# Optimization experiments

Hardware: AMD Instinct MI355X
Metric: run time of the kernel (lower is better)

The kernel has to match this reference:

```python
import jax, jax.numpy as jnp
import numpy as np
import math

B, N, DIN, H, D, M, K, E = 1, 30000, 128, 4, 64, 64, 6, 480000
TAU = 0.25
EPS = 1e-6  # numerical_stabilizer in softmax_kernel_transformation


def _make_projection(m, d, seed=0):
    # FAVOR+ projection: stacked QR-orthogonalized blocks, rows rescaled by
    # norms of iid gaussian rows (scaling == 0 branch of create_projection_matrix).
    rng = np.random.default_rng(seed)
    blocks, rows = [], 0
    while rows < m:
        q, _ = np.linalg.qr(rng.standard_normal((d, d)))
        blocks.append(q.T[: min(d, m - rows)])
        rows += d
    mat = np.vstack(blocks)
    mult = np.linalg.norm(rng.standard_normal((m, d)), axis=1)
    return jnp.asarray(mult[:, None] * mat, dtype=jnp.float32)


def setup_inputs() -> dict:
    key = jax.random.key(0)
    ks = jax.random.split(key, 10)
    f32 = jnp.float32
    return {
        "z": jax.random.normal(ks[0], (B, N, DIN), dtype=f32),
        "Wq_w": jax.random.normal(ks[1], (DIN, H * D), dtype=f32) * DIN ** -0.5,
        "Wq_b": jnp.zeros((H * D,), f32),
        "Wk_w": jax.random.normal(ks[2], (DIN, H * D), dtype=f32) * DIN ** -0.5,
        "Wk_b": jnp.zeros((H * D,), f32),
        "Wv_w": jax.random.normal(ks[3], (DIN, H * D), dtype=f32) * DIN ** -0.5,
        "Wv_b": jnp.zeros((H * D,), f32),
        "Wo_w": jax.random.normal(ks[4], (H * D, D), dtype=f32) * (H * D) ** -0.5,
        "Wo_b": jnp.zeros((D,), f32),
        "proj": _make_projection(M, D),
        "gumbels": jax.random.gumbel(ks[5], (N, B, H, K), dtype=f32),
        "edge_index": jax.random.randint(ks[6], (2, E), 0, N),
    }


def _softmax_kernel(data, proj, is_query):
    # softmax_kernel_transformation: positive random features for exp kernel.
    dn = 1.0 / jnp.sqrt(jnp.sqrt(jnp.asarray(data.shape[-1], data.dtype)))
    data = data * dn  # [B,N,H,D]
    ratio = 1.0 / jnp.sqrt(jnp.asarray(proj.shape[0], data.dtype))
    dd = jnp.einsum("bnhd,md->bnhm", data, proj)
    diag = jnp.sum(data * data, axis=-1, keepdims=True) * 0.5
    if is_query:
        mx = jnp.max(dd, axis=-1, keepdims=True)            # per-row max
    else:
        mx = jnp.max(dd, axis=(1, 3), keepdims=True)        # max over n and m
    return ratio * (jnp.exp(dd - diag - mx) + EPS)


def reference(z, Wq_w, Wq_b, Wk_w, Wk_b, Wv_w, Wv_b, Wo_w, Wo_b, proj, gumbels, edge_index):
    inv_sqrt_tau = 1.0 / math.sqrt(TAU)
    q = (z @ Wq_w + Wq_b).reshape(B, N, H, D) * inv_sqrt_tau
    k = (z @ Wk_w + Wk_b).reshape(B, N, H, D) * inv_sqrt_tau
    v = (z @ Wv_w + Wv_b).reshape(B, N, H, D)

    qp = jnp.transpose(_softmax_kernel(q, proj, True), (1, 0, 2, 3))   # [N,B,H,M]
    kp = jnp.transpose(_softmax_kernel(k, proj, False), (1, 0, 2, 3))  # [N,B,H,M]
    v = jnp.transpose(v, (1, 0, 2, 3))                                  # [N,B,H,D]

    g = gumbels / TAU                                                   # [N,B,H,K]
    kt = kp[:, :, :, None, :] * jnp.exp(g)[..., None]                   # [N,B,H,K,M]

    kvs = jnp.einsum("nbhkm,nbhd->bhkmd", kt, v)
    z_num = jnp.einsum("nbhm,bhkmd->nbhkd", qp, kvs)                    # [N,B,H,K,D]
    ks_sum = jnp.sum(kt, axis=0)                                        # [B,H,K,M]
    z_den = jnp.einsum("nbhm,bhkm->nbhk", qp, ks_sum)                   # [N,B,H,K]
    z_out = jnp.mean(z_num / z_den[..., None], axis=3)                  # [N,B,H,D]
    z_out = jnp.transpose(z_out, (1, 0, 2, 3))                          # [B,N,H,D]

    # edge attention weights (for edge loss), non-gumbel normalizer
    start, end = edge_index[0], edge_index[1]
    edge_num = jnp.einsum("ebhm,ebhm->ebh", qp[end], kp[start])         # [E,B,H]
    norm = jnp.einsum("nbhm,bhm->nbh", qp, jnp.sum(kp, axis=0))         # [N,B,H]
    A_weight = jnp.transpose(edge_num / norm[end], (1, 0, 2))           # [B,E,H]

    z_next = z_out.reshape(B, N, H * D) @ Wo_w + Wo_b                   # [B,N,D]
    return z_next, A_weight
```

## Files before the change

kernel.cpp:

```cpp
#include <hip/hip_runtime.h>
#include <hip/hip_bf16.h>

#define NN   30000
#define DIN  128
#define NHD  256
#define HH   4
#define DD   64
#define MM   64
#define KK   6
#define EE   480000
#define ZOFF 1920000
#define NCS   125
#define CHUNK 240
#define PITCH  30208
#define PITCH4 3776

typedef __attribute__((ext_vector_type(8))) short bf16x8;
typedef __attribute__((ext_vector_type(4))) float f32x4;
typedef __attribute__((ext_vector_type(2))) float f32x2;

__device__ __forceinline__ unsigned f2key(float f) {
    unsigned u = __float_as_uint(f);
    return (u & 0x80000000u) ? ~u : (u | 0x80000000u);
}
__device__ __forceinline__ float key2f(unsigned k) {
    return __uint_as_float((k & 0x80000000u) ? (k ^ 0x80000000u) : ~k);
}
__device__ __forceinline__ unsigned short f2bf(float f) {
    unsigned u = __float_as_uint(f);
    unsigned r = ((u >> 16) & 1u) + 0x7fffu;
    return (unsigned short)((u + r) >> 16);
}
__device__ __forceinline__ float bf2f(unsigned short u) {
    return __uint_as_float((unsigned)u << 16);
}
__device__ __forceinline__ unsigned char ftofp8(float x) {
    unsigned u = __float_as_uint(x);
    int e32 = (int)(u >> 23) - 127;
    if (e32 <= -7) {
        int m = (int)rintf(x * 512.f);
        return (unsigned char)m;
    }
    unsigned r = ((u >> 20) & 1u) + 0x7FFFFu;
    u += r;
    e32 = (int)(u >> 23) - 127;
    if (e32 > 8) return 0x7E;
    int m = (u >> 20) & 7;
    return (unsigned char)(((e32 + 7) << 3) | m);
}
__device__ __forceinline__ float fp8tof(unsigned char u) {
    int e = (u >> 3) & 15, m = u & 7;
    if (e == 0) return (float)m * 0.001953125f;
    return __uint_as_float((unsigned)((e + 120) << 23) | ((unsigned)m << 20));
}
__device__ __forceinline__ void fp8x4tof(unsigned w, float* o) {
#if __has_builtin(__builtin_amdgcn_cvt_pk_f32_fp8)
    f32x2 lo = __builtin_amdgcn_cvt_pk_f32_fp8((int)w, false);
    f32x2 hi = __builtin_amdgcn_cvt_pk_f32_fp8((int)w, true);
    o[0] = lo[0]; o[1] = lo[1]; o[2] = hi[0]; o[3] = hi[1];
#else
    o[0] = fp8tof((unsigned char)(w & 255));
    o[1] = fp8tof((unsigned char)((w >> 8) & 255));
    o[2] = fp8tof((unsigned char)((w >> 16) & 255));
    o[3] = fp8tof((unsigned char)((w >> 24) & 255));
#endif
}

__global__ void init_kernel(unsigned* gmax) {
    if (threadIdx.x < HH) gmax[threadIdx.x] = 0u;
}

__global__ __launch_bounds__(256) void zcast_kernel(
    const float* __restrict__ z, unsigned short* __restrict__ zh) {
    int idx = blockIdx.x * 256 + threadIdx.x;
    float4 v = ((const float4*)z)[idx];
    ushort4 u;
    u.x = f2bf(v.x); u.y = f2bf(v.y); u.z = f2bf(v.z); u.w = f2bf(v.w);
    ((ushort4*)zh)[idx] = u;
}

__global__ __launch_bounds__(256) void wtransp_kernel(
    const float* __restrict__ Wq, const float* __restrict__ Wk,
    const float* __restrict__ Wv, unsigned short* __restrict__ WT) {
    __shared__ unsigned short tl[64][72];
    const int t = threadIdx.x;
    const int kt = blockIdx.x & 1, ct = blockIdx.x >> 1;
    const int wi = blockIdx.y;
    const float* W = (wi == 0) ? Wq : (wi == 1) ? Wk : Wv;
    const float4* W4 = (const float4*)W;
    #pragma unroll
    for (int it = 0; it < 4; ++it) {
        int idx = t + it * 256;
        int r = idx >> 4, c4 = idx & 15;
        float4 v = W4[(kt * 64 + r) * 64 + ct * 16 + c4];
        tl[c4 * 4 + 0][r] = f2bf(v.x);
        tl[c4 * 4 + 1][r] = f2bf(v.y);
        tl[c4 * 4 + 2][r] = f2bf(v.z);
        tl[c4 * 4 + 3][r] = f2bf(v.w);
    }
    __syncthreads();
    uint4* d4 = (uint4*)WT;
    #pragma unroll
    for (int it = 0; it < 2; ++it) {
        int idx = t + it * 256;
        int m = idx >> 3, g = idx & 7;
        d4[((size_t)wi * 256 + ct * 64 + m) * 16 + kt * 8 + g] = *(uint4*)&tl[m][g * 8];
    }
}

__global__ void projcast_kernel(const float* __restrict__ proj,
                                unsigned short* __restrict__ projh) {
    int i = blockIdx.x * 256 + threadIdx.x;
    projh[i] = f2bf(proj[i] * 0.35355339059327373f);
}

__global__ __launch_bounds__(256) void qkv_mfma_kernel(
    const unsigned short* __restrict__ zh, const unsigned short* __restrict__ WT,
    const float* __restrict__ bq, const float* __restrict__ bk, const float* __restrict__ bv,
    unsigned short* __restrict__ qh, unsigned short* __restrict__ kh,
    unsigned short* __restrict__ vh) {
    __shared__ __align__(16) unsigned short zt[128 * 128];
    __shared__ __align__(16) unsigned short wt[64 * 128];
    const int t = threadIdx.x;
    const int n0 = blockIdx.x * 128;
    const int wi = blockIdx.y;
    const float sc = (wi == 2) ? 1.0f : 2.0f;
    const float* bias = (wi == 0) ? bq : (wi == 1) ? bk : bv;
    unsigned short* outp = (wi == 0) ? qh : (wi == 1) ? kh : vh;
    const uint4* zg = (const uint4*)zh;
    #pragma unroll
    for (int it = 0; it < 8; ++it) {
        int idx = t + it * 256;
        int row = idx >> 4, g = idx & 15;
        int n = n0 + row;
        uint4 v = make_uint4(0u, 0u, 0u, 0u);
        if (n < NN) v = zg[(size_t)n * 16 + g];
        *(uint4*)&zt[row * 128 + ((g ^ (row & 7)) * 8)] = v;
    }
    const uint4* wg = (const uint4*)WT + (size_t)wi * 4096;
    const int w = t >> 6, lane = t & 63, lrow = lane & 15, lk = lane >> 4;
    for (int cc = 0; cc < 4; ++cc) {
        __syncthreads();
        #pragma unroll
        for (int it = 0; it < 4; ++it) {
            int idx = t + it * 256;
            int r = idx >> 4, g = idx & 15;
            *(uint4*)&wt[r * 128 + ((g ^ (r & 7)) * 8)] = wg[(cc * 64 + r) * 16 + g];
        }
        __syncthreads();
        f32x4 acc[4][2];
        #pragma unroll
        for (int mt = 0; mt < 4; ++mt) {
            acc[mt][0] = (f32x4){0.f, 0.f, 0.f, 0.f};
            acc[mt][1] = (f32x4){0.f, 0.f, 0.f, 0.f};
        }
        #pragma unroll
        for (int ks = 0; ks < 4; ++ks) {
            const int g0 = ks * 4 + lk;
            bf16x8 a[4], b[2];
            #pragma unroll
            for (int mt = 0; mt < 4; ++mt) {
                int r = mt * 16 + lrow;
                a[mt] = *(const bf16x8*)&wt[r * 128 + ((g0 ^ (r & 7)) * 8)];
            }
            #pragma unroll
            for (int nt = 0; nt < 2; ++nt) {
                int node = (w * 2 + nt) * 16 + lrow;
                b[nt] = *(const bf16x8*)&zt[node * 128 + ((g0 ^ (node & 7)) * 8)];
            }
            #pragma unroll
            for (int mt = 0; mt < 4; ++mt)
                #pragma unroll
                for (int nt = 0; nt < 2; ++nt)
                    acc[mt][nt] = __builtin_amdgcn_mfma_f32_16x16x32_bf16(
                        a[mt], b[nt], acc[mt][nt], 0, 0, 0);
        }
        #pragma unroll
        for (int mt = 0; mt < 4; ++mt) {
            int cbase = cc * 64 + mt * 16 + lk * 4;
            float4 bi = *(const float4*)&bias[cbase];
            #pragma unroll
            for (int nt = 0; nt < 2; ++nt) {
                int n = n0 + (w * 2 + nt) * 16 + lrow;
                if (n < NN) {
                    ushort4 u;
                    u.x = f2bf((acc[mt][nt][0] + bi.x) * sc);
                    u.y = f2bf((acc[mt][nt][1] + bi.y) * sc);
                    u.z = f2bf((acc[mt][nt][2] + bi.z) * sc);
                    u.w = f2bf((acc[mt][nt][3] + bi.w) * sc);
                    *(ushort4*)&outp[(size_t)n * NHD + cbase] = u;
                }
            }
        }
    }
}

__global__ __launch_bounds__(256) void feat_mfma_kernel(
    unsigned short* __restrict__ qbh, const unsigned short* __restrict__ kh,
    float* __restrict__ kb, const unsigned short* __restrict__ projh,
    unsigned* __restrict__ gmax) {
    __shared__ __align__(16) unsigned short at[64 * 64];
    __shared__ __align__(16) unsigned short pb[64 * 64];
    __shared__ __align__(16) float ddt[64 * 68];
    __shared__ float diag_sh[64];
    __shared__ float wmax_sh[4];
    const int t = threadIdx.x;
    const int h = blockIdx.y;
    const int n0 = blockIdx.x * 64;
    const int tx = t & 15, ty = t >> 4;
    const uint4* pg = (const uint4*)projh;
    #pragma unroll
    for (int q = 0; q < 2; ++q) {
        int idx = t + q * 256;
        int m = idx >> 3, g = idx & 7;
        *(uint4*)&pb[m * 64 + ((g ^ (m & 7)) * 8)] = pg[idx];
    }
    const int w = t >> 6, lane = t & 63, lrow = lane & 15, lk = lane >> 4;
    const int arow = w * 16 + lrow;
    #pragma unroll
    for (int pass = 0; pass < 2; ++pass) {
        const uint4* src = (const uint4*)(pass ? kh : qbh);
        __syncthreads();
        #pragma unroll
        for (int q = 0; q < 2; ++q) {
            int idx = t + q * 256;
            int n = idx >> 3, g = idx & 7;
            uint4 v = make_uint4(0u, 0u, 0u, 0u);
            if (n0 + n < NN) v = src[(size_t)(n0 + n) * 32 + h * 8 + g];
            *(uint4*)&at[n * 64 + ((g ^ (n & 7)) * 8)] = v;
            const unsigned short* e8 = (const unsigned short*)&v;
            float ss = 0.f;
            #pragma unroll
            for (int j2 = 0; j2 < 8; ++j2) { float f = bf2f(e8[j2]); ss += f * f; }
            ss += __shfl_xor(ss, 1, 64);
            ss += __shfl_xor(ss, 2, 64);
            ss += __shfl_xor(ss, 4, 64);
            if (g == 0) diag_sh[n] = 0.0625f * ss;
        }
        __syncthreads();
        bf16x8 a0 = *(const bf16x8*)&at[arow * 64 + ((lk ^ (arow & 7)) * 8)];
        bf16x8 a1 = *(const bf16x8*)&at[arow * 64 + (((lk + 4) ^ (arow & 7)) * 8)];
        #pragma unroll
        for (int ct = 0; ct < 4; ++ct) {
            int brow = ct * 16 + lrow;
            bf16x8 b0 = *(const bf16x8*)&pb[brow * 64 + ((lk ^ (brow & 7)) * 8)];
            bf16x8 b1 = *(const bf16x8*)&pb[brow * 64 + (((lk + 4) ^ (brow & 7)) * 8)];
            f32x4 acc = {0.f, 0.f, 0.f, 0.f};
            acc = __builtin_amdgcn_mfma_f32_16x16x32_bf16(a0, b0, acc, 0, 0, 0);
            acc = __builtin_amdgcn_mfma_f32_16x16x32_bf16(a1, b1, acc, 0, 0, 0);
            #pragma unroll
            for (int r = 0; r < 4; ++r)
                ddt[(w * 16 + lk * 4 + r) * 68 + ct * 16 + lrow] = acc[r];
        }
        __syncthreads();
        if (pass == 0) {
            #pragma unroll
            for (int i = 0; i < 4; ++i) {
                int n = n0 + ty * 4 + i;
                float a_[4];
                #pragma unroll
                for (int j = 0; j < 4; ++j) a_[j] = ddt[(ty * 4 + i) * 68 + tx * 4 + j];
                float mx = fmaxf(fmaxf(a_[0], a_[1]), fmaxf(a_[2], a_[3]));
                mx = fmaxf(mx, __shfl_xor(mx, 1, 64));
                mx = fmaxf(mx, __shfl_xor(mx, 2, 64));
                mx = fmaxf(mx, __shfl_xor(mx, 4, 64));
                mx = fmaxf(mx, __shfl_xor(mx, 8, 64));
                if (n < NN) {
                    float dg = diag_sh[ty * 4 + i] + mx;
                    ushort4 u;
                    u.x = f2bf(0.125f * (__expf(a_[0] - dg) + 1e-6f));
                    u.y = f2bf(0.125f * (__expf(a_[1] - dg) + 1e-6f));
                    u.z = f2bf(0.125f * (__expf(a_[2] - dg) + 1e-6f));
                    u.w = f2bf(0.125f * (__expf(a_[3] - dg) + 1e-6f));
                    *(ushort4*)&qbh[(size_t)n * NHD + h * DD + tx * 4] = u;
                }
            }
        } else {
            float km = -3.4e38f;
            #pragma unroll
            for (int i = 0; i < 4; ++i) {
                int n = n0 + ty * 4 + i;
                if (n < NN) {
                    float a_[4];
                    #pragma unroll
                    for (int j = 0; j < 4; ++j) a_[j] = ddt[(ty * 4 + i) * 68 + tx * 4 + j];
                    float dg = diag_sh[ty * 4 + i];
                    float4 o;
                    o.x = a_[0] - dg; o.y = a_[1] - dg;
                    o.z = a_[2] - dg; o.w = a_[3] - dg;
                    *(float4*)&kb[(size_t)n * NHD + h * DD + tx * 4] = o;
                    km = fmaxf(km, fmaxf(fmaxf(a_[0], a_[1]), fmaxf(a_[2], a_[3])));
                }
            }
            #pragma unroll
            for (int off = 1; off < 64; off <<= 1) km = fmaxf(km, __shfl_xor(km, off, 64));
            if ((t & 63) == 0) wmax_sh[t >> 6] = km;
            __syncthreads();
            if (t == 0) {
                float m2 = fmaxf(fmaxf(wmax_sh[0], wmax_sh[1]), fmaxf(wmax_sh[2], wmax_sh[3]));
                atomicMax(&gmax[h], f2key(m2));
            }
        }
    }
}

__global__ __launch_bounds__(256) void kfin_tr_kernel(
    const float* __restrict__ kb, const unsigned* __restrict__ gmax,
    unsigned short* __restrict__ kbh, unsigned short* __restrict__ kbhT) {
    __shared__ unsigned short tl[64][72];
    const int t = threadIdx.x;
    const int n0 = blockIdx.x * 64;
    const int h = blockIdx.y;
    const float mx = key2f(gmax[h]);
    const float4* s4 = (const float4*)kb;
    #pragma unroll
    for (int it = 0; it < 4; ++it) {
        int idx = t + it * 256;
        int n = idx >> 4, c4 = idx & 15;
        ushort4 u = make_ushort4(0, 0, 0, 0);
        if (n0 + n < NN) {
            float4 v = s4[(size_t)(n0 + n) * 64 + h * 16 + c4];
            u.x = f2bf(0.125f * (__expf(v.x - mx) + 1e-6f));
            u.y = f2bf(0.125f * (__expf(v.y - mx) + 1e-6f));
            u.z = f2bf(0.125f * (__expf(v.z - mx) + 1e-6f));
            u.w = f2bf(0.125f * (__expf(v.w - mx) + 1e-6f));
            *(ushort4*)&kbh[(size_t)(n0 + n) * NHD + h * DD + c4 * 4] = u;
        }
        tl[c4 * 4 + 0][n] = u.x;
        tl[c4 * 4 + 1][n] = u.y;
        tl[c4 * 4 + 2][n] = u.z;
        tl[c4 * 4 + 3][n] = u.w;
    }
    __syncthreads();
    uint4* d4 = (uint4*)kbhT;
    #pragma unroll
    for (int it = 0; it < 2; ++it) {
        int idx = t + it * 256;
        int m = idx >> 3, g = idx & 7;
        d4[(size_t)(h * 64 + m) * PITCH4 + (n0 >> 3) + g] = *(uint4*)&tl[m][g * 8];
    }
}

__global__ __launch_bounds__(256) void transp_bf16_kernel(
    const unsigned short* __restrict__ src, unsigned short* __restrict__ dst) {
    __shared__ unsigned short tl[64][72];
    const int t = threadIdx.x;
    const int nt = blockIdx.x * 64;
    const int h = blockIdx.y;
    const uint4* s4 = (const uint4*)src;
    #pragma unroll
    for (int it = 0; it < 2; ++it) {
        int idx = t + it * 256;
        int n = idx >> 3, g = idx & 7;
        uint4 v = make_uint4(0u, 0u, 0u, 0u);
        if (nt + n < NN) v = s4[(size_t)(nt + n) * 32 + h * 8 + g];
        const unsigned short* e = (const unsigned short*)&v;
        #pragma unroll
        for (int j = 0; j < 8; ++j) tl[g * 8 + j][n] = e[j];
    }
    __syncthreads();
    uint4* d4 = (uint4*)dst;
    #pragma unroll
    for (int it = 0; it < 2; ++it) {
        int idx = t + it * 256;
        int m = idx >> 3, g = idx & 7;
        d4[(size_t)(h * 64 + m) * PITCH4 + (nt >> 3) + g] = *(uint4*)&tl[m][g * 8];
    }
}

__global__ __launch_bounds__(256) void fp8cast_kernel(
    const unsigned short* __restrict__ src, unsigned char* __restrict__ dst) {
    int idx = blockIdx.x * 256 + threadIdx.x;
    uint4 v = ((const uint4*)src)[idx];
    const unsigned short* e = (const unsigned short*)&v;
    unsigned char o[8];
    #pragma unroll
    for (int j = 0; j < 8; ++j) o[j] = ftofp8(bf2f(e[j]) * 2048.f);
    ((uint2*)dst)[idx] = *(uint2*)o;
}

__global__ __launch_bounds__(512) void kvs_kernel(
    const unsigned short* __restrict__ kbhT, const unsigned short* __restrict__ vbhT,
    const float* __restrict__ gum,
    unsigned short* __restrict__ kvsp, float* __restrict__ ksp, float* __restrict__ ksump) {
    __shared__ __align__(16) unsigned short va [64 * 64];
    __shared__ __align__(16) unsigned short kpw[KK][64 * 64];
    __shared__ float w_sh[KK][256];
    const int c = blockIdx.x, h = blockIdx.y;
    const int t = threadIdx.x;
    const int n0 = c * CHUNK;
    const int n1 = n0 + CHUNK;
    for (int i = t; i < 256; i += 512) {
        int n = n0 + i;
        bool ok = (i < CHUNK);
        #pragma unroll
        for (int k = 0; k < KK; ++k)
            w_sh[k][i] = ok ? __expf(gum[n * 24 + h * KK + k] * 4.0f) : 0.f;
    }
    const int m_ = t >> 3, g_ = t & 7;
    const int w = t >> 6, lane = t & 63, lrow = lane & 15, lk = lane >> 4;
    const int ds = w & 3, mh = w >> 2;
    const int arow = ds * 16 + lrow;
    f32x4 acc[KK][2];
    #pragma unroll
    for (int k = 0; k < KK; ++k) {
        acc[k][0] = (f32x4){0.f, 0.f, 0.f, 0.f};
        acc[k][1] = (f32x4){0.f, 0.f, 0.f, 0.f};
    }
    float ks_acc[KK] = {0.f, 0.f, 0.f, 0.f, 0.f, 0.f};
    float ksum_acc = 0.f;
    const uint4* kT4 = (const uint4*)kbhT;
    const uint4* vT4 = (const uint4*)vbhT;
    __syncthreads();
    #pragma unroll
    for (int s = 0; s < 4; ++s) {
        const int nb = n0 + s * 64;
        uint4 kvv = kT4[(size_t)(h * 64 + m_) * PITCH4 + (nb >> 3) + g_];
        uint4 vvv = vT4[(size_t)(h * 64 + m_) * PITCH4 + (nb >> 3) + g_];
        const int slot = g_ ^ (m_ & 7);
        *(uint4*)&va[m_ * 64 + slot * 8] = vvv;
        float kf[8];
        {
            const unsigned short* ke = (const unsigned short*)&kvv;
            float sl = 0.f;
            int nbase = nb + g_ * 8;
            #pragma unroll
            for (int e = 0; e < 8; ++e) {
                kf[e] = bf2f(ke[e]);
                if (nbase + e < n1) sl += kf[e];
            }
            sl += __shfl_xor(sl, 1, 64);
            sl += __shfl_xor(sl, 2, 64);
            sl += __shfl_xor(sl, 4, 64);
            if (g_ == 0) ksum_acc += sl;
        }
        const int bw = s * 64;
        const int gg = g_ ^ (m_ & 7);
        #pragma unroll
        for (int k = 0; k < KK; ++k) {
            unsigned short ov[8];
            float sl = 0.f;
            #pragma unroll
            for (int e = 0; e < 8; ++e) {
                float p = kf[e] * w_sh[k][bw + gg * 8 + e];
                sl += p;
                ov[e] = f2bf(p);
            }
            *(uint4*)&kpw[k][m_ * 64 + g_ * 8] = *(uint4*)ov;
            sl += __shfl_xor(sl, 1, 64);
            sl += __shfl_xor(sl, 2, 64);
            sl += __shfl_xor(sl, 4, 64);
            if (g_ == 0) ks_acc[k] += sl;
        }
        __syncthreads();
        bf16x8 a0 = *(const bf16x8*)&va[arow * 64 + ((lk ^ (arow & 7)) * 8)];
        bf16x8 a1 = *(const bf16x8*)&va[arow * 64 + (((lk + 4) ^ (arow & 7)) * 8)];
        #pragma unroll
        for (int k = 0; k < KK; ++k) {
            #pragma unroll
            for (int mt = 0; mt < 2; ++mt) {
                int m = (mh * 2 + mt) * 16 + lrow;
                bf16x8 b0 = *(const bf16x8*)&kpw[k][m * 64 + ((lk ^ (m & 7)) * 8)];
                bf16x8 b1 = *(const bf16x8*)&kpw[k][m * 64 + (((lk + 4) ^ (m & 7)) * 8)];
                acc[k][mt] = __builtin_amdgcn_mfma_f32_16x16x32_bf16(a0, b0, acc[k][mt], 0, 0, 0);
                acc[k][mt] = __builtin_amdgcn_mfma_f32_16x16x32_bf16(a1, b1, acc[k][mt], 0, 0, 0);
            }
        }
        __syncthreads();
    }
    const size_t cb = (size_t)(c * HH + h) * KK;
    #pragma unroll
    for (int k = 0; k < KK; ++k)
        #pragma unroll
        for (int mt = 0; mt < 2; ++mt) {
            int m = (mh * 2 + mt) * 16 + lrow;
            #pragma unroll
            for (int r = 0; r < 4; ++r) {
                int d = ds * 16 + lk * 4 + r;
                kvsp[(cb + k) * 4096 + d * 64 + m] = f2bf(acc[k][mt][r]);
            }
        }
    if (g_ == 0) {
        #pragma unroll
        for (int k = 0; k < KK; ++k)
            ksp[(cb + k) * 64 + m_] = ks_acc[k];
        ksump[(size_t)(c * HH + h) * 64 + m_] = ksum_acc;
    }
}

__global__ void reduce_kernel(const unsigned short* __restrict__ kvsp,
                              const float* __restrict__ ksp, const float* __restrict__ ksump,
                              unsigned short* __restrict__ kvshT, float* __restrict__ kss,
                              float* __restrict__ ksum) {
    int idx = blockIdx.x * 256 + threadIdx.x;
    if (idx < 98304) {
        float s = 0.f;
        for (int c = 0; c < NCS; ++c) s += bf2f(kvsp[c * 98304 + idx]);
        kvshT[idx] = f2bf(s);
    } else if (idx < 98304 + 1536) {
        int o = idx - 98304;
        float s = 0.f;
        for (int c = 0; c < NCS; ++c) s += ksp[c * 1536 + o];
        kss[o] = s;
    } else if (idx < 98304 + 1536 + 256) {
        int o = idx - 98304 - 1536;
        float s = 0.f;
        for (int c = 0; c < NCS; ++c) s += ksump[c * 256 + o];
        ksum[o] = s;
    }
}

__global__ __launch_bounds__(256) void znum_kernel(
    const unsigned short* __restrict__ qbh, const unsigned short* __restrict__ kvshT,
    const float* __restrict__ kss, const float* __restrict__ ksum,
    unsigned short* __restrict__ zouth, float* __restrict__ nrm) {
    __shared__ __align__(16) unsigned short qpa[64 * 64];
    __shared__ __align__(16) unsigned short bt[6 * 64 * 64];
    __shared__ float ks_sh[384];
    __shared__ float ksum_sh[64];
    __shared__ float zdi[64 * 6];
    const int t = threadIdx.x;
    const int h = blockIdx.y;
    const int n0 = blockIdx.x * 64;
    const uint4* qg = (const uint4*)qbh;
    #pragma unroll
    for (int q = 0; q < 2; ++q) {
        int idx = t + q * 256;
        int row = idx >> 3, c8 = idx & 7;
        int n = n0 + row;
        uint4 v = make_uint4(0u, 0u, 0u, 0u);
        if (n < NN) v = qg[n * 32 + h * 8 + c8];
        *(uint4*)&qpa[row * 64 + ((c8 ^ (row & 7)) * 8)] = v;
    }
    const uint4* bg = (const uint4*)kvshT;
    #pragma unroll
    for (int q = 0; q < 12; ++q) {
        int idx = t + q * 256;
        int kd = idx >> 3, c8 = idx & 7;
        *(uint4*)&bt[kd * 64 + ((c8 ^ (kd & 7)) * 8)] = bg[h * 3072 + idx];
    }
    for (int i = t; i < 384; i += 256) ks_sh[i] = kss[h * 384 + i];
    if (t < 64) ksum_sh[t] = ksum[h * 64 + t];
    __syncthreads();
    for (int idx = t; idx < 512; idx += 256) {
        if (idx < 384) {
            int node = idx / 6, k = idx - node * 6;
            int swz = (node & 7) << 3;
            float s = 0.f;
            for (int m = 0; m < 64; ++m)
                s += bf2f(qpa[node * 64 + (m ^ swz)]) * ks_sh[k * 64 + m];
            zdi[node * 6 + k] = 1.0f / s;
        } else if (idx < 448) {
            int node = idx - 384;
            int swz = (node & 7) << 3;
            float s = 0.f;
            for (int m = 0; m < 64; ++m)
                s += bf2f(qpa[node * 64 + (m ^ swz)]) * ksum_sh[m];
            int n = n0 + node;
            if (n < NN) nrm[n * HH + h] = s;
        }
    }
    __syncthreads();
    const int w = t >> 6, lane = t & 63;
    const int lrow = lane & 15, lk = lane >> 4;
    const int arow = w * 16 + lrow;
    const int aswz = (arow & 7) << 3;
    bf16x8 a0 = *(const bf16x8*)&qpa[arow * 64 + ((lk * 8) ^ aswz)];
    bf16x8 a1 = *(const bf16x8*)&qpa[arow * 64 + ((lk * 8 + 32) ^ aswz)];
    const float inv6 = 1.0f / 6.0f;
    #pragma unroll
    for (int dt = 0; dt < 4; ++dt) {
        f32x4 outv = {0.f, 0.f, 0.f, 0.f};
        #pragma unroll
        for (int k = 0; k < KK; ++k) {
            int kd = k * 64 + dt * 16 + lrow;
            int sw = (kd & 7) << 3;
            bf16x8 b0 = *(const bf16x8*)&bt[kd * 64 + ((lk * 8) ^ sw)];
            bf16x8 b1 = *(const bf16x8*)&bt[kd * 64 + ((lk * 8 + 32) ^ sw)];
            f32x4 acc = {0.f, 0.f, 0.f, 0.f};
            acc = __builtin_amdgcn_mfma_f32_16x16x32_bf16(a0, b0, acc, 0, 0, 0);
            acc = __builtin_amdgcn_mfma_f32_16x16x32_bf16(a1, b1, acc, 0, 0, 0);
            #pragma unroll
            for (int r = 0; r < 4; ++r)
                outv[r] += zdi[(w * 16 + lk * 4 + r) * 6 + k] * acc[r];
        }
        #pragma unroll
        for (int r = 0; r < 4; ++r) {
            int n = n0 + w * 16 + lk * 4 + r;
            if (n < NN) zouth[(size_t)n * NHD + h * DD + dt * 16 + lrow] = f2bf(outv[r] * inv6);
        }
    }
}

__global__ __launch_bounds__(256) void outproj_kernel(
    const unsigned short* __restrict__ zouth, const float* __restrict__ Wo,
    const float* __restrict__ bo, float* __restrict__ out) {
    __shared__ float zsh[16][NHD];
    const int t = threadIdx.x;
    const int n0 = blockIdx.x * 16;
    const uint4* zg = (const uint4*)zouth;
    #pragma unroll
    for (int q = 0; q < 2; ++q) {
        int idx = t + q * 256;
        int row = idx >> 5, g = idx & 31;
        uint4 v = zg[(size_t)(n0 + row) * 32 + g];
        const unsigned short* e = (const unsigned short*)&v;
        #pragma unroll
        for (int j = 0; j < 8; ++j) zsh[row][g * 8 + j] = bf2f(e[j]);
    }
    __syncthreads();
    const int c = t & 63, g = t >> 6;
    float acc[4];
    #pragma unroll
    for (int i = 0; i < 4; ++i) acc[i] = bo[c];
    for (int r = 0; r < 256; ++r) {
        float w = Wo[r * 64 + c];
        #pragma unroll
        for (int i = 0; i < 4; ++i) acc[i] += zsh[g + 4 * i][r] * w;
    }
    #pragma unroll
    for (int i = 0; i < 4; ++i)
        out[(n0 + g + 4 * i) * 64 + c] = acc[i];
}

__global__ __launch_bounds__(256) void edge_fp8_kernel(
    const unsigned char* __restrict__ qb8, const unsigned char* __restrict__ kb8,
    const int* __restrict__ ei, const float* __restrict__ nrm,
    float* __restrict__ out) {
    const int t = threadIdx.x;
    const int li = t & 15;
    const int e = blockIdx.x * 16 + (t >> 4);
    const int s = ei[e], d = ei[EE + e];
    uint4 qv = ((const uint4*)qb8)[d * 16 + li];
    uint4 kv = ((const uint4*)kb8)[s * 16 + li];
    float qf[16], kf[16];
    fp8x4tof(qv.x, qf + 0);  fp8x4tof(qv.y, qf + 4);
    fp8x4tof(qv.z, qf + 8);  fp8x4tof(qv.w, qf + 12);
    fp8x4tof(kv.x, kf + 0);  fp8x4tof(kv.y, kf + 4);
    fp8x4tof(kv.z, kf + 8);  fp8x4tof(kv.w, kf + 12);
    float p = 0.f;
    #pragma unroll
    for (int i = 0; i < 16; ++i) p = fmaf(qf[i], kf[i], p);
    p += __shfl_xor(p, 1, 64);
    p += __shfl_xor(p, 2, 64);
    if ((li & 3) == 0) {
        int h = li >> 2;
        out[ZOFF + e * 4 + h] = p * (1.0f / (2048.f * 2048.f)) / nrm[d * HH + h];
    }
}

extern "C" void kernel_launch(void* const* d_in, const int* in_sizes, int n_in,
                              void* d_out, int out_size, void* d_ws, size_t ws_size,
                              hipStream_t stream) {
    (void)in_sizes; (void)n_in; (void)out_size;
    const float* z  = (const float*)d_in[0];
    const float* Wq = (const float*)d_in[1];
    const float* bq = (const float*)d_in[2];
    const float* Wk = (const float*)d_in[3];
    const float* bk = (const float*)d_in[4];
    const float* Wv = (const float*)d_in[5];
    const float* bv = (const float*)d_in[6];
    const float* Wo = (const float*)d_in[7];
    const float* bo = (const float*)d_in[8];
    const float* proj = (const float*)d_in[9];
    const float* gum  = (const float*)d_in[10];
    const int*   ei   = (const int*)d_in[11];
    float* out = (float*)d_out;
    float* ws = (float*)d_ws;

    if (ws_size / 4 < (size_t)38673348) return;

    float* kb    = ws + 7680000;
    unsigned char* qb8 = (unsigned char*)(ws + 7680000);
    unsigned char* kb8 = (unsigned char*)(ws + 9600000);
    unsigned short* zouth = (unsigned short*)(ws + 15360000);
    unsigned short* vh = (unsigned short*)(ws + 15360000);
    unsigned short* kvshT = (unsigned short*)(ws + 23040000);
    unsigned short* projh = (unsigned short*)(ws + 23089152);
    float* kss   = ws + 23138304;
    float* ksum  = ws + 23139840;
    float* nrm   = ws + 23140096;
    unsigned* gmax = (unsigned*)(ws + 23260096);
    unsigned short* qbh = (unsigned short*)(ws + 23260100);
    unsigned short* kbh = (unsigned short*)(ws + 27100100);
    unsigned short* kbhT = (unsigned short*)(ws + 30940100);
    unsigned short* vbhT = (unsigned short*)(ws + 34806724);
    unsigned short* zh = (unsigned short*)ws;
    unsigned short* WT = (unsigned short*)(ws + 3840000);
    float* ksp   = ws;
    float* ksump = ws + 192000;
    unsigned short* kvsp = (unsigned short*)(ws + 224000);

    init_kernel<<<1, 64, 0, stream>>>(gmax);
    zcast_kernel<<<3750, 256, 0, stream>>>(z, zh);
    wtransp_kernel<<<dim3(8, 3), 256, 0, stream>>>(Wq, Wk, Wv, WT);
    projcast_kernel<<<16, 256, 0, stream>>>(proj, projh);
    qkv_mfma_kernel<<<dim3(235, 3), 256, 0, stream>>>(zh, WT, bq, bk, bv, qbh, kbh, vh);
    transp_bf16_kernel<<<dim3(472, HH), 256, 0, stream>>>(vh, vbhT);
    feat_mfma_kernel<<<dim3(469, HH), 256, 0, stream>>>(qbh, kbh, kb, projh, gmax);
    kfin_tr_kernel<<<dim3(472, HH), 256, 0, stream>>>(kb, gmax, kbh, kbhT);
    fp8cast_kernel<<<3750, 256, 0, stream>>>(qbh, qb8);
    fp8cast_kernel<<<3750, 256, 0, stream>>>(kbh, kb8);
    kvs_kernel<<<dim3(NCS, HH), 512, 0, stream>>>(kbhT, vbhT, gum, kvsp, ksp, ksump);
    reduce_kernel<<<392, 256, 0, stream>>>(kvsp, ksp, ksump, kvshT, kss, ksum);
    znum_kernel<<<dim3(469, HH), 256, 0, stream>>>(qbh, kvshT, kss, ksum, zouth, nrm);
    outproj_kernel<<<1875, 256, 0, stream>>>(zouth, Wo, bo, out);
    edge_fp8_kernel<<<30000, 256, 0, stream>>>(qb8, kb8, ei, nrm, out);
}
```

Measured before the change: 226.6 us.

## Compute znum denominators with MFMA, use 512 threads, prefetch kvs loads

The znum kernel's scalar loops that computed the per-node denominators and normalizers are replaced by an MFMA product against a small bf16 matrix of ks sums. The block grows to 512 threads, with the d-tiles split across two wave halves. Separately, kvs_kernel now issues the next chunk's k/v global loads one step early to hide latency. The trade is that the denominators are now computed from bf16-rounded ks sums, which costs some precision, and the extra syncthreads and larger block may reduce occupancy.

```diff
diff --git a/kernel.cpp b/kernel.cpp
--- a/kernel.cpp
+++ b/kernel.cpp
@@ -411,12 +411,12 @@
     float ksum_acc = 0.f;
     const uint4* kT4 = (const uint4*)kbhT;
     const uint4* vT4 = (const uint4*)vbhT;
+    uint4 kvv = kT4[(size_t)(h * 64 + m_) * PITCH4 + (n0 >> 3) + g_];
+    uint4 vvv = vT4[(size_t)(h * 64 + m_) * PITCH4 + (n0 >> 3) + g_];
     __syncthreads();
     #pragma unroll
     for (int s = 0; s < 4; ++s) {
         const int nb = n0 + s * 64;
-        uint4 kvv = kT4[(size_t)(h * 64 + m_) * PITCH4 + (nb >> 3) + g_];
-        uint4 vvv = vT4[(size_t)(h * 64 + m_) * PITCH4 + (nb >> 3) + g_];
         const int slot = g_ ^ (m_ & 7);
         *(uint4*)&va[m_ * 64 + slot * 8] = vvv;
         float kf[8];
@@ -433,6 +433,11 @@
             sl += __shfl_xor(sl, 2, 64);
             sl += __shfl_xor(sl, 4, 64);
             if (g_ == 0) ksum_acc += sl;
+        }
+        if (s < 3) {
+            const int nb2 = nb + 64;
+            kvv = kT4[(size_t)(h * 64 + m_) * PITCH4 + (nb2 >> 3) + g_];
+            vvv = vT4[(size_t)(h * 64 + m_) * PITCH4 + (nb2 >> 3) + g_];
         }
         const int bw = s * 64;
         const int gg = g_ ^ (m_ & 7);
@@ -510,23 +515,20 @@
     }
 }
 
-__global__ __launch_bounds__(256) void znum_kernel(
+__global__ __launch_bounds__(512) void znum_kernel(
     const unsigned short* __restrict__ qbh, const unsigned short* __restrict__ kvshT,
     const float* __restrict__ kss, const float* __restrict__ ksum,
     unsigned short* __restrict__ zouth, float* __restrict__ nrm) {
     __shared__ __align__(16) unsigned short qpa[64 * 64];
     __shared__ __align__(16) unsigned short bt[6 * 64 * 64];
-    __shared__ float ks_sh[384];
-    __shared__ float ksum_sh[64];
+    __shared__ __align__(16) unsigned short bbuf[16 * 72];
     __shared__ float zdi[64 * 6];
     const int t = threadIdx.x;
     const int h = blockIdx.y;
     const int n0 = blockIdx.x * 64;
     const uint4* qg = (const uint4*)qbh;
-    #pragma unroll
-    for (int q = 0; q < 2; ++q) {
-        int idx = t + q * 256;
-        int row = idx >> 3, c8 = idx & 7;
+    {
+        int row = t >> 3, c8 = t & 7;
         int n = n0 + row;
         uint4 v = make_uint4(0u, 0u, 0u, 0u);
         if (n < NN) v = qg[n * 32 + h * 8 + c8];
@@ -534,42 +536,49 @@
     }
     const uint4* bg = (const uint4*)kvshT;
     #pragma unroll
-    for (int q = 0; q < 12; ++q) {
-        int idx = t + q * 256;
+    for (int q = 0; q < 6; ++q) {
+        int idx = t + q * 512;
         int kd = idx >> 3, c8 = idx & 7;
         *(uint4*)&bt[kd * 64 + ((c8 ^ (kd & 7)) * 8)] = bg[h * 3072 + idx];
     }
-    for (int i = t; i < 384; i += 256) ks_sh[i] = kss[h * 384 + i];
-    if (t < 64) ksum_sh[t] = ksum[h * 64 + t];
-    __syncthreads();
-    for (int idx = t; idx < 512; idx += 256) {
-        if (idx < 384) {
-            int node = idx / 6, k = idx - node * 6;
-            int swz = (node & 7) << 3;
-            float s = 0.f;
-            for (int m = 0; m < 64; ++m)
-                s += bf2f(qpa[node * 64 + (m ^ swz)]) * ks_sh[k * 64 + m];
-            zdi[node * 6 + k] = 1.0f / s;
-        } else if (idx < 448) {
-            int node = idx - 384;
-            int swz = (node & 7) << 3;
-            float s = 0.f;
-            for (int m = 0; m < 64; ++m)
-                s += bf2f(qpa[node * 64 + (m ^ swz)]) * ksum_sh[m];
-            int n = n0 + node;
-            if (n < NN) nrm[n * HH + h] = s;
-        }
+    #pragma unroll
+    for (int q = 0; q < 2; ++q) {
+        int idx = t + q * 512;
+        int col = idx >> 6, m = idx & 63;
+        float v = 0.f;
+        if (col < 6) v = kss[h * 384 + col * 64 + m];
+        else if (col == 6) v = ksum[h * 64 + m];
+        bbuf[col * 72 + m] = f2bf(v);
     }
     __syncthreads();
     const int w = t >> 6, lane = t & 63;
     const int lrow = lane & 15, lk = lane >> 4;
-    const int arow = w * 16 + lrow;
+    const int w2 = w & 3, wh = w >> 2;
+    const int arow = w2 * 16 + lrow;
     const int aswz = (arow & 7) << 3;
     bf16x8 a0 = *(const bf16x8*)&qpa[arow * 64 + ((lk * 8) ^ aswz)];
     bf16x8 a1 = *(const bf16x8*)&qpa[arow * 64 + ((lk * 8 + 32) ^ aswz)];
+    if (wh == 0) {
+        bf16x8 b0 = *(const bf16x8*)&bbuf[lrow * 72 + lk * 8];
+        bf16x8 b1 = *(const bf16x8*)&bbuf[lrow * 72 + lk * 8 + 32];
+        f32x4 acc = {0.f, 0.f, 0.f, 0.f};
+        acc = __builtin_amdgcn_mfma_f32_16x16x32_bf16(a0, b0, acc, 0, 0, 0);
+        acc = __builtin_amdgcn_mfma_f32_16x16x32_bf16(a1, b1, acc, 0, 0, 0);
+        #pragma unroll
+        for (int r = 0; r < 4; ++r) {
+            int node = w2 * 16 + lk * 4 + r;
+            if (lrow < 6) zdi[node * 6 + lrow] = 1.0f / acc[r];
+            else if (lrow == 6) {
+                int n = n0 + node;
+                if (n < NN) nrm[n * HH + h] = acc[r];
+            }
+        }
+    }
+    __syncthreads();
     const float inv6 = 1.0f / 6.0f;
     #pragma unroll
-    for (int dt = 0; dt < 4; ++dt) {
+    for (int dtt = 0; dtt < 2; ++dtt) {
+        const int dt = wh * 2 + dtt;
         f32x4 outv = {0.f, 0.f, 0.f, 0.f};
         #pragma unroll
         for (int k = 0; k < KK; ++k) {
@@ -582,11 +591,11 @@
             acc = __builtin_amdgcn_mfma_f32_16x16x32_bf16(a1, b1, acc, 0, 0, 0);
             #pragma unroll
             for (int r = 0; r < 4; ++r)
-                outv[r] += zdi[(w * 16 + lk * 4 + r) * 6 + k] * acc[r];
+                outv[r] += zdi[(w2 * 16 + lk * 4 + r) * 6 + k] * acc[r];
         }
         #pragma unroll
         for (int r = 0; r < 4; ++r) {
-            int n = n0 + w * 16 + lk * 4 + r;
+            int n = n0 + w2 * 16 + lk * 4 + r;
             if (n < NN) zouth[(size_t)n * NHD + h * DD + dt * 16 + lrow] = f2bf(outv[r] * inv6);
         }
     }
@@ -703,7 +712,7 @@
     fp8cast_kernel<<<3750, 256, 0, stream>>>(kbh, kb8);
     kvs_kernel<<<dim3(NCS, HH), 512, 0, stream>>>(kbhT, vbhT, gum, kvsp, ksp, ksump);
     reduce_kernel<<<392, 256, 0, stream>>>(kvsp, ksp, ksump, kvshT, kss, ksum);
-    znum_kernel<<<dim3(469, HH), 256, 0, stream>>>(qbh, kvshT, kss, ksum, zouth, nrm);
+    znum_kernel<<<dim3(469, HH), 512, 0, stream>>>(qbh, kvshT, kss, ksum, zouth, nrm);
     outproj_kernel<<<1875, 256, 0, stream>>>(zouth, Wo, bo, out);
     edge_fp8_kernel<<<30000, 256, 0, stream>>>(qb8, kb8, ei, nrm, out);
 }
```

After: 214.9 us. 5.1% less time.
